# Kernel optimization log

Hardware: AMD Instinct MI355X
Metric: run time of the kernel (lower is better)

## Reference

```python
import jax, jax.numpy as jnp
import numpy as np

D_MODEL = 1024
N_HEADS = 16
HEAD_DIM = D_MODEL // N_HEADS  # 64


def setup_inputs() -> dict:
    key = jax.random.key(0)
    k1, k2, k3 = jax.random.split(key, 3)
    x = jax.random.normal(k1, (2, 2048, D_MODEL), dtype=jnp.float32)
    # nn.Linear(d, 3d, bias=False): store transposed so y = x @ W
    w_qkv = jax.random.normal(k2, (D_MODEL, 3 * D_MODEL), dtype=jnp.float32) * (D_MODEL ** -0.5)
    w_proj = jax.random.normal(k3, (D_MODEL, D_MODEL), dtype=jnp.float32) * (D_MODEL ** -0.5)
    return {"x": x, "w_qkv": w_qkv, "w_proj": w_proj}


def reference(x, w_qkv, w_proj):
    b, n, _ = x.shape
    qkv = x @ w_qkv  # [b, n, 3*d_model]
    # einops 'b n (h d qkv) -> qkv b h n d': qkv axis is innermost of the split
    qkv = qkv.reshape(b, n, N_HEADS, HEAD_DIM, 3)
    q = jnp.moveaxis(qkv[..., 0], 1, 2)  # [b, h, n, d]
    k = jnp.moveaxis(qkv[..., 1], 1, 2)
    v = jnp.moveaxis(qkv[..., 2], 1, 2)
    scale = HEAD_DIM ** -0.5
    scores = jnp.einsum('bhqd,bhkd->bhqk', q, k) * scale  # [b, h, n, n]
    causal = jnp.tril(jnp.ones((n, n), dtype=bool))
    scores = jnp.where(causal[None, None], scores, -jnp.inf)
    attn = jax.nn.softmax(scores, axis=-1)
    out = jnp.einsum('bhqk,bhkd->bhqd', attn, v)  # [b, h, n, d]
    out = jnp.moveaxis(out, 1, 2).reshape(b, n, D_MODEL)  # 'b h n d -> b n (h d)'
    return out @ w_proj
```

## Files before the change

### kernel.cpp

```cpp
#include <hip/hip_runtime.h>
#include <cstdint>
#include <cstddef>

#define D_MODEL 1024
#define N_HEADS 16
#define HEAD_DIM 64
#define SEQ 2048
#define BATCH 2

typedef __attribute__((ext_vector_type(8))) short bf16x8;
typedef __attribute__((ext_vector_type(4))) float f32x4;

__device__ inline unsigned short f2bf(float f) {
    union { float f; unsigned u; } v; v.f = f;
    unsigned r = v.u + 0x7fffu + ((v.u >> 16) & 1u);
    return (unsigned short)(r >> 16);
}

__device__ __forceinline__ unsigned cvtpk_bf16(float lo, float hi) {
    unsigned r;
    asm("v_cvt_pk_bf16_f32 %0, %1, %2" : "=v"(r) : "v"(lo), "v"(hi));
    return r;
}
__device__ __forceinline__ unsigned short f2bf_hw(float f) {
    return (unsigned short)cvtpk_bf16(f, 0.f);
}

__device__ __forceinline__ void gload_lds16(const unsigned short* g, unsigned short* l) {
    __builtin_amdgcn_global_load_lds(
        (const __attribute__((address_space(1))) unsigned int*)g,
        (__attribute__((address_space(3))) unsigned int*)l, 16, 0, 0);
}

#define WAITCNT_VM4 0x0F74
#define WAITCNT_VM0 0x0F70

__global__ __launch_bounds__(256) void fused_convert_kernel(
    const float* __restrict__ X, unsigned short* __restrict__ Xb,
    const float* __restrict__ Wq, unsigned short* __restrict__ Wqt,
    const float* __restrict__ Wp, unsigned short* __restrict__ Wpt)
{
    const int blk = blockIdx.x;
    const int tid = threadIdx.x;
    __shared__ float t[32][33];

    if (blk < 2048) {
        const int idx = blk * 256 + tid;
        const float4* src = (const float4*)X;
        float4 v0 = src[idx * 2], v1 = src[idx * 2 + 1];
        uint4 o;
        o.x = cvtpk_bf16(v0.x, v0.y);
        o.y = cvtpk_bf16(v0.z, v0.w);
        o.z = cvtpk_bf16(v1.x, v1.y);
        o.w = cvtpk_bf16(v1.z, v1.w);
        ((uint4*)Xb)[idx] = o;
    } else if (blk < 5120) {
        const int bb = blk - 2048;
        const int c0 = (bb % 96) * 32, r0 = (bb / 96) * 32;
        const int a = tid & 31, b = tid >> 5;
#pragma unroll
        for (int i = 0; i < 32; i += 8)
            t[b + i][a] = Wq[(size_t)(r0 + b + i) * (3 * D_MODEL) + c0 + a];
        __syncthreads();
#pragma unroll
        for (int i = 0; i < 32; i += 8) {
            const int c = c0 + b + i;
            const int which = c % 3;
            const int np = which * 1024 + c / 3;
            const float s = (which == 0) ? 0.125f : 1.0f;
            Wqt[(size_t)np * D_MODEL + r0 + a] = f2bf_hw(t[a][b + i] * s);
        }
    } else {
        const int bb = blk - 5120;
        const int c0 = (bb % 32) * 32, r0 = (bb / 32) * 32;
        const int a = tid & 31, b = tid >> 5;
#pragma unroll
        for (int i = 0; i < 32; i += 8)
            t[b + i][a] = Wp[(size_t)(r0 + b + i) * D_MODEL + c0 + a];
        __syncthreads();
#pragma unroll
        for (int i = 0; i < 32; i += 8)
            Wpt[(size_t)(c0 + b + i) * D_MODEL + r0 + a] = f2bf_hw(t[a][b + i]);
    }
}

__global__ __launch_bounds__(256) void v_transpose(
    const unsigned short* __restrict__ V, unsigned short* __restrict__ Vt)
{
    const int n0 = blockIdx.x * 64;
    const int bh = blockIdx.y;
    __shared__ unsigned short t[64 * 72];
    const int tid = threadIdx.x;
    const uint4* src = (const uint4*)(V + ((size_t)bh * SEQ + n0) * HEAD_DIM);
#pragma unroll
    for (int it = 0; it < 2; it++) {
        const int lin = tid + it * 256;
        const int row = lin >> 3, p = lin & 7;
        ((uint4*)t)[row * 9 + p] = src[lin];
    }
    __syncthreads();
#pragma unroll
    for (int it = 0; it < 2; it++) {
        const int lin = tid + it * 256;
        const int drow = lin >> 3, p = lin & 7;
        union { unsigned short u[8]; uint4 v; } o;
#pragma unroll
        for (int e = 0; e < 8; e++) o.u[e] = t[(p * 8 + e) * 72 + drow];
        ((uint4*)(Vt + ((size_t)bh * HEAD_DIM + drow) * SEQ + n0))[p] = o.v;
    }
}

#define GEMM_PIPE3_BODY(A_, B_, KBASE, NITER)                                  \
    const int tid = threadIdx.x;                                               \
    const int w = tid >> 6, lane = tid & 63;                                   \
    const int l15 = lane & 15, quad = lane >> 4;                               \
    const int wr = w >> 1, wc = w & 1;                                         \
    const int row0 = blockIdx.y * 128, col0 = blockIdx.x * 128;                \
    __shared__ unsigned short As[3][4096];                                     \
    __shared__ unsigned short Bs[3][4096];                                     \
    const f32x4 zero4 = {0.f, 0.f, 0.f, 0.f};                                  \
    f32x4 acc[4][4];                                                           \
    _Pragma("unroll") for (int i = 0; i < 4; i++)                              \
        _Pragma("unroll") for (int j = 0; j < 4; j++) acc[i][j] = zero4;       \
    auto stage_ = [&](int sb_, int kt_) {                                      \
        const int k0 = (KBASE) + kt_ * 32 + quad * 8;                          \
        _Pragma("unroll") for (int i = 0; i < 2; i++) {                        \
            const int f = w * 2 + i;                                           \
            gload_lds16((A_) + (size_t)(row0 + f * 16 + l15) * D_MODEL + k0,   \
                        &As[sb_][f * 512 + lane * 8]);                         \
            gload_lds16((B_) + (size_t)(col0 + f * 16 + l15) * D_MODEL + k0,   \
                        &Bs[sb_][f * 512 + lane * 8]);                         \
        }                                                                      \
    };                                                                         \
    stage_(0, 0);                                                              \
    stage_(1, 1);                                                              \
    int sb = 0;                                                                \
    for (int kt = 0; kt < (NITER); kt++) {                                     \
        if (kt < (NITER) - 1) {                                                \
            __builtin_amdgcn_s_waitcnt(WAITCNT_VM4);                           \
            __builtin_amdgcn_s_barrier();                                      \
            if (kt + 2 < (NITER)) stage_((sb + 2 > 2) ? sb - 1 : sb + 2, kt + 2); \
        } else {                                                               \
            __builtin_amdgcn_s_waitcnt(WAITCNT_VM0);                           \
            __builtin_amdgcn_s_barrier();                                      \
        }                                                                      \
        bf16x8 af[4], bfr[4];                                                  \
        _Pragma("unroll") for (int i = 0; i < 4; i++)                          \
            af[i] = *(const bf16x8*)&As[sb][(wr * 4 + i) * 512 + lane * 8];    \
        _Pragma("unroll") for (int j = 0; j < 4; j++)                          \
            bfr[j] = *(const bf16x8*)&Bs[sb][(wc * 4 + j) * 512 + lane * 8];   \
        _Pragma("unroll") for (int i = 0; i < 4; i++)                          \
            _Pragma("unroll") for (int j = 0; j < 4; j++)                      \
                acc[i][j] = __builtin_amdgcn_mfma_f32_16x16x32_bf16(           \
                    af[i], bfr[j], acc[i][j], 0, 0, 0);                        \
        sb = (sb == 2) ? 0 : sb + 1;                                           \
    }

__global__ __launch_bounds__(256) void gemm_qkv_mfma(
    const unsigned short* __restrict__ A, const unsigned short* __restrict__ B,
    unsigned short* __restrict__ Q, unsigned short* __restrict__ Kq,
    unsigned short* __restrict__ Vb)
{
    GEMM_PIPE3_BODY(A, B, 0, 32)
    const int nbase = col0 + wc * 64;
    const int which = nbase >> 10;
    unsigned short* const dst = (which == 0) ? Q : (which == 1) ? Kq : Vb;
#pragma unroll
    for (int i = 0; i < 4; i++) {
        const int rowb = row0 + wr * 64 + i * 16 + quad * 4;
        const int bb = rowb >> 11, n = rowb & (SEQ - 1);
#pragma unroll
        for (int rp = 0; rp < 2; rp++) {
#pragma unroll
            for (int j = 0; j < 4; j++) {
                const unsigned u = cvtpk_bf16(acc[i][j][2 * rp], acc[i][j][2 * rp + 1]);
                const int idx = (nbase + j * 16 + l15) & 1023;
                const int h = idx >> 6, dd = idx & 63;
                unsigned short* p =
                    dst + (((size_t)(bb * N_HEADS + h)) * SEQ + n + 2 * rp) * HEAD_DIM + dd;
                p[0] = (unsigned short)u;
                p[HEAD_DIM] = (unsigned short)(u >> 16);
            }
        }
    }
}

__global__ __launch_bounds__(256) void gemm_proj_splitk(
    const unsigned short* __restrict__ A, const unsigned short* __restrict__ B,
    float* __restrict__ P)
{
    const int kbase = blockIdx.z * 512;
    GEMM_PIPE3_BODY(A, B, kbase, 16)
    float* const dst = P + (size_t)blockIdx.z * (4096ull * 1024ull);
#pragma unroll
    for (int i = 0; i < 4; i++) {
#pragma unroll
        for (int r = 0; r < 4; r++) {
            const int row = row0 + wr * 64 + i * 16 + quad * 4 + r;
#pragma unroll
            for (int j = 0; j < 4; j++) {
                const int c = col0 + wc * 64 + j * 16 + l15;
                dst[(size_t)row * D_MODEL + c] = acc[i][j][r];
            }
        }
    }
}

__global__ __launch_bounds__(256) void add_out_kernel(
    const float* __restrict__ P, float* __restrict__ out)
{
    const float4* p0 = (const float4*)P;
    const float4* p1 = (const float4*)(P + 4096ull * 1024ull);
    float4* o = (float4*)out;
    const int base = (blockIdx.x * 256 + threadIdx.x) * 4;
#pragma unroll
    for (int j = 0; j < 4; j++) {
        float4 a = p0[base + j], b = p1[base + j];
        float4 r = {a.x + b.x, a.y + b.y, a.z + b.z, a.w + b.w};
        o[base + j] = r;
    }
}

__global__ __launch_bounds__(256) void flash_attn_kernel(
    const unsigned short* __restrict__ Q,
    const unsigned short* __restrict__ K,
    const unsigned short* __restrict__ Vt,
    unsigned short* __restrict__ O)
{
    const int idx = blockIdx.x;
    const int bh = idx & 31;
    const int qt2 = idx >> 5;
    const int hi = qt2 >> 3, lo = qt2 & 7;
    const int qt = (hi == 0) ? lo : (hi == 1) ? 31 - lo : (hi == 2) ? lo + 8 : 23 - lo;

    const int tid = threadIdx.x;
    const int w = tid >> 6, lane = tid & 63;
    const int l15 = lane & 15, quad = lane >> 4;

    __shared__ unsigned short Ks[2][4096];
    __shared__ unsigned short Vs[2][4096];
    __shared__ unsigned short Ps[4][1024];

    bf16x8 qf[2];
    {
        const unsigned short* qrow =
            Q + ((size_t)bh * SEQ + qt * 64 + w * 16 + l15) * HEAD_DIM;
        qf[0] = *(const bf16x8*)(qrow + quad * 8);
        qf[1] = *(const bf16x8*)(qrow + 32 + quad * 8);
    }

    const f32x4 zero4 = {0.f, 0.f, 0.f, 0.f};
    f32x4 o_acc[4] = {zero4, zero4, zero4, zero4};
    float m_i = -1e30f, l_i = 0.f;

    auto stage = [&](int bf, int kt_t) {
        const int key0 = kt_t * 64;
#pragma unroll
        for (int i = 0; i < 2; i++) {
            const int f = w * 2 + i;
            const int ct = f >> 1, kh = f & 1;
            gload_lds16(K + ((size_t)bh * SEQ + key0 + ct * 16 + l15) * HEAD_DIM
                          + kh * 32 + quad * 8,
                        &Ks[bf][f * 512 + lane * 8]);
            gload_lds16(Vt + ((size_t)bh * HEAD_DIM + ct * 16 + l15) * SEQ
                           + key0 + kh * 32 + quad * 8,
                        &Vs[bf][f * 512 + lane * 8]);
        }
    };

    stage(0, 0);
    int buf = 0;

    const int qg = qt * 64 + w * 16 + l15;

    for (int kt = 0; kt <= qt; kt++) {
        __syncthreads();
        if (kt < qt) stage(buf ^ 1, kt + 1);

        f32x4 st[4] = {zero4, zero4, zero4, zero4};
        __builtin_amdgcn_s_setprio(1);
#pragma unroll
        for (int kh = 0; kh < 2; kh++) {
#pragma unroll
            for (int ct = 0; ct < 4; ct++) {
                bf16x8 kf = *(const bf16x8*)&Ks[buf][(ct * 2 + kh) * 512 + lane * 8];
                st[ct] = __builtin_amdgcn_mfma_f32_16x16x32_bf16(kf, qf[kh], st[ct], 0, 0, 0);
            }
        }
        __builtin_amdgcn_s_setprio(0);

        float mt = -1e30f;
        if (kt == qt) {
#pragma unroll
            for (int ct = 0; ct < 4; ct++) {
#pragma unroll
                for (int r = 0; r < 4; r++) {
                    const int kg = kt * 64 + ct * 16 + quad * 4 + r;
                    float v = (kg > qg) ? -1e30f : st[ct][r];
                    st[ct][r] = v;
                    mt = fmaxf(mt, v);
                }
            }
        } else {
#pragma unroll
            for (int ct = 0; ct < 4; ct++)
#pragma unroll
                for (int r = 0; r < 4; r++)
                    mt = fmaxf(mt, st[ct][r]);
        }
        mt = fmaxf(mt, __shfl_xor(mt, 16));
        mt = fmaxf(mt, __shfl_xor(mt, 32));

        float mn = m_i;
        if (!__all(mt <= m_i + 8.0f)) {
            mn = fmaxf(m_i, mt);
            const float alpha = __expf(m_i - mn);
            m_i = mn;
            l_i *= alpha;
            float ar[4];
#pragma unroll
            for (int r = 0; r < 4; r++)
                ar[r] = __shfl(alpha, (lane & 48) | (quad * 4 + r));
#pragma unroll
            for (int dt = 0; dt < 4; dt++)
#pragma unroll
                for (int r = 0; r < 4; r++)
                    o_acc[dt][r] *= ar[r];
        }

        float ls = 0.f;
#pragma unroll
        for (int ct = 0; ct < 4; ct++) {
            const float p0 = __expf(st[ct][0] - mn);
            const float p1 = __expf(st[ct][1] - mn);
            const float p2 = __expf(st[ct][2] - mn);
            const float p3 = __expf(st[ct][3] - mn);
            ls += (p0 + p1) + (p2 + p3);
            uint2 pk2;
            pk2.x = cvtpk_bf16(p0, p1);
            pk2.y = cvtpk_bf16(p2, p3);
            const int addr = (ct >> 1) * 512 + ((ct & 1) * 2 + (quad >> 1)) * 128
                           + l15 * 8 + (quad & 1) * 4;
            *(uint2*)&Ps[w][addr] = pk2;
        }
        l_i += ls;

        __builtin_amdgcn_s_setprio(1);
#pragma unroll
        for (int kh = 0; kh < 2; kh++) {
            bf16x8 pa = *(const bf16x8*)&Ps[w][kh * 512 + quad * 128 + l15 * 8];
#pragma unroll
            for (int dt = 0; dt < 4; dt++) {
                bf16x8 vf = *(const bf16x8*)&Vs[buf][(dt * 2 + kh) * 512 + lane * 8];
                o_acc[dt] = __builtin_amdgcn_mfma_f32_16x16x32_bf16(pa, vf, o_acc[dt], 0, 0, 0);
            }
        }
        __builtin_amdgcn_s_setprio(0);
        buf ^= 1;
    }

    l_i += __shfl_xor(l_i, 16);
    l_i += __shfl_xor(l_i, 32);
    const float linv = 1.0f / l_i;
    float lr[4];
#pragma unroll
    for (int r = 0; r < 4; r++)
        lr[r] = __shfl(linv, (lane & 48) | (quad * 4 + r));

    const int b = bh >> 4, h = bh & 15;
#pragma unroll
    for (int r = 0; r < 4; r++) {
        const int q = qt * 64 + w * 16 + quad * 4 + r;
        unsigned short* orow = O + ((size_t)b * SEQ + q) * D_MODEL + h * HEAD_DIM;
#pragma unroll
        for (int dt = 0; dt < 4; dt++)
            orow[dt * 16 + l15] = f2bf_hw(o_acc[dt][r] * lr[r]);
    }
}

extern "C" void kernel_launch(void* const* d_in, const int* in_sizes, int n_in,
                              void* d_out, int out_size, void* d_ws, size_t ws_size,
                              hipStream_t stream) {
    const float* x      = (const float*)d_in[0];
    const float* w_qkv  = (const float*)d_in[1];
    const float* w_proj = (const float*)d_in[2];
    float* out = (float*)d_out;

    unsigned short* Xb  = (unsigned short*)d_ws;
    unsigned short* Wqt = Xb  + (size_t)4 * 1024 * 1024;
    unsigned short* Wpt = Wqt + (size_t)3 * 1024 * 1024;
    unsigned short* Qb  = Wpt + (size_t)1 * 1024 * 1024;
    unsigned short* Kb  = Qb  + (size_t)4 * 1024 * 1024;
    unsigned short* Vb  = Kb  + (size_t)4 * 1024 * 1024;
    unsigned short* Vtb = Vb  + (size_t)4 * 1024 * 1024;
    unsigned short* Ob  = Vtb + (size_t)4 * 1024 * 1024;

    float* Pp = (float*)Qb;

    fused_convert_kernel<<<dim3(6144), 256, 0, stream>>>(
        x, Xb, w_qkv, Wqt, w_proj, Wpt);

    gemm_qkv_mfma<<<dim3(3 * D_MODEL / 128, BATCH * SEQ / 128), 256, 0, stream>>>(
        Xb, Wqt, Qb, Kb, Vb);

    v_transpose<<<dim3(SEQ / 64, BATCH * N_HEADS), 256, 0, stream>>>(Vb, Vtb);

    flash_attn_kernel<<<dim3(SEQ / 64 * BATCH * N_HEADS), 256, 0, stream>>>(
        Qb, Kb, Vtb, Ob);

    gemm_proj_splitk<<<dim3(D_MODEL / 128, BATCH * SEQ / 128, 2), 256, 0, stream>>>(
        Ob, Wpt, Pp);

    add_out_kernel<<<dim3(1024), 256, 0, stream>>>(Pp, out);
}
```

Baseline: 217.2 us.

## Retile GEMMs to 128x64 with 2 waves, double buffering, XCD-aware block swizzle

Both GEMMs change from 128x128 tiles with 4 waves and a 3-stage LDS pipeline to 128x64 tiles with 2 waves (each wave owns 64 rows) and a 2-stage double buffer. Block indices are remapped so each XCD gets a contiguous region of the output grid for better L2 locality. The smaller tile and LDS footprint are meant to raise occupancy and block count and to simplify the per-head epilogue. In exchange, each tile reuses less data, and waiting on all outstanding loads every iteration reduces load/compute overlap.

```diff
diff --git a/kernel.cpp b/kernel.cpp
--- a/kernel.cpp
+++ b/kernel.cpp
@@ -32,7 +32,6 @@
         (__attribute__((address_space(3))) unsigned int*)l, 16, 0, 0);
 }
 
-#define WAITCNT_VM4 0x0F74
 #define WAITCNT_VM0 0x0F70
 
 __global__ __launch_bounds__(256) void fused_convert_kernel(
@@ -110,74 +109,72 @@
     }
 }
 
-#define GEMM_PIPE3_BODY(A_, B_, KBASE, NITER)                                  \
+#define GEMM_PIPE2_BODY(A_, B_, KBASE, NITER, BX_, BY_)                        \
     const int tid = threadIdx.x;                                               \
     const int w = tid >> 6, lane = tid & 63;                                   \
     const int l15 = lane & 15, quad = lane >> 4;                               \
-    const int wr = w >> 1, wc = w & 1;                                         \
-    const int row0 = blockIdx.y * 128, col0 = blockIdx.x * 128;                \
-    __shared__ unsigned short As[3][4096];                                     \
-    __shared__ unsigned short Bs[3][4096];                                     \
+    const int row0 = (BY_) * 128, col0 = (BX_) * 64;                           \
+    __shared__ unsigned short SM_[12288];     \
     const f32x4 zero4 = {0.f, 0.f, 0.f, 0.f};                                  \
     f32x4 acc[4][4];                                                           \
     _Pragma("unroll") for (int i = 0; i < 4; i++)                              \
         _Pragma("unroll") for (int j = 0; j < 4; j++) acc[i][j] = zero4;       \
     auto stage_ = [&](int sb_, int kt_) {                                      \
         const int k0 = (KBASE) + kt_ * 32 + quad * 8;                          \
+        _Pragma("unroll") for (int i = 0; i < 4; i++) {                        \
+            const int f = w * 4 + i;                                           \
+            gload_lds16((A_) + (size_t)(row0 + f * 16 + l15) * D_MODEL + k0,   \
+                        &SM_[sb_ * 4096 + f * 512 + lane * 8]);                \
+        }                                                                      \
         _Pragma("unroll") for (int i = 0; i < 2; i++) {                        \
-            const int f = w * 2 + i;                                           \
-            gload_lds16((A_) + (size_t)(row0 + f * 16 + l15) * D_MODEL + k0,   \
-                        &As[sb_][f * 512 + lane * 8]);                         \
-            gload_lds16((B_) + (size_t)(col0 + f * 16 + l15) * D_MODEL + k0,   \
-                        &Bs[sb_][f * 512 + lane * 8]);                         \
+            const int g = w * 2 + i;                                           \
+            gload_lds16((B_) + (size_t)(col0 + g * 16 + l15) * D_MODEL + k0,   \
+                        &SM_[8192 + sb_ * 2048 + g * 512 + lane * 8]);         \
         }                                                                      \
     };                                                                         \
     stage_(0, 0);                                                              \
-    stage_(1, 1);                                                              \
     int sb = 0;                                                                \
     for (int kt = 0; kt < (NITER); kt++) {                                     \
-        if (kt < (NITER) - 1) {                                                \
-            __builtin_amdgcn_s_waitcnt(WAITCNT_VM4);                           \
-            __builtin_amdgcn_s_barrier();                                      \
-            if (kt + 2 < (NITER)) stage_((sb + 2 > 2) ? sb - 1 : sb + 2, kt + 2); \
-        } else {                                                               \
-            __builtin_amdgcn_s_waitcnt(WAITCNT_VM0);                           \
-            __builtin_amdgcn_s_barrier();                                      \
-        }                                                                      \
+        __builtin_amdgcn_s_waitcnt(WAITCNT_VM0);                               \
+        __builtin_amdgcn_s_barrier();                                          \
+        if (kt + 1 < (NITER)) stage_(sb ^ 1, kt + 1);                          \
         bf16x8 af[4], bfr[4];                                                  \
         _Pragma("unroll") for (int i = 0; i < 4; i++)                          \
-            af[i] = *(const bf16x8*)&As[sb][(wr * 4 + i) * 512 + lane * 8];    \
+            af[i] = *(const bf16x8*)&SM_[sb * 4096 + (w * 4 + i) * 512 + lane * 8]; \
         _Pragma("unroll") for (int j = 0; j < 4; j++)                          \
-            bfr[j] = *(const bf16x8*)&Bs[sb][(wc * 4 + j) * 512 + lane * 8];   \
+            bfr[j] = *(const bf16x8*)&SM_[8192 + sb * 2048 + j * 512 + lane * 8];   \
         _Pragma("unroll") for (int i = 0; i < 4; i++)                          \
             _Pragma("unroll") for (int j = 0; j < 4; j++)                      \
                 acc[i][j] = __builtin_amdgcn_mfma_f32_16x16x32_bf16(           \
                     af[i], bfr[j], acc[i][j], 0, 0, 0);                        \
-        sb = (sb == 2) ? 0 : sb + 1;                                           \
-    }
-
-__global__ __launch_bounds__(256) void gemm_qkv_mfma(
+        sb ^= 1;                                                               \
+    }
+
+__global__ __launch_bounds__(128) void gemm_qkv_mfma(
     const unsigned short* __restrict__ A, const unsigned short* __restrict__ B,
     unsigned short* __restrict__ Q, unsigned short* __restrict__ Kq,
     unsigned short* __restrict__ Vb)
 {
-    GEMM_PIPE3_BODY(A, B, 0, 32)
-    const int nbase = col0 + wc * 64;
-    const int which = nbase >> 10;
+    const int lin = blockIdx.x + 48 * blockIdx.y;
+    const int xcd = lin & 7, t = lin >> 3;
+    const int bx = (xcd & 1) * 24 + t % 24;
+    const int by = (xcd >> 1) * 8 + t / 24;
+    GEMM_PIPE2_BODY(A, B, 0, 32, bx, by)
+    const int which = col0 >> 10;
+    const int hloc = (col0 >> 6) & 15;
     unsigned short* const dst = (which == 0) ? Q : (which == 1) ? Kq : Vb;
 #pragma unroll
     for (int i = 0; i < 4; i++) {
-        const int rowb = row0 + wr * 64 + i * 16 + quad * 4;
+        const int rowb = row0 + w * 64 + i * 16 + quad * 4;
         const int bb = rowb >> 11, n = rowb & (SEQ - 1);
 #pragma unroll
         for (int rp = 0; rp < 2; rp++) {
 #pragma unroll
             for (int j = 0; j < 4; j++) {
                 const unsigned u = cvtpk_bf16(acc[i][j][2 * rp], acc[i][j][2 * rp + 1]);
-                const int idx = (nbase + j * 16 + l15) & 1023;
-                const int h = idx >> 6, dd = idx & 63;
+                const int dd = j * 16 + l15;
                 unsigned short* p =
-                    dst + (((size_t)(bb * N_HEADS + h)) * SEQ + n + 2 * rp) * HEAD_DIM + dd;
+                    dst + (((size_t)(bb * N_HEADS + hloc)) * SEQ + n + 2 * rp) * HEAD_DIM + dd;
                 p[0] = (unsigned short)u;
                 p[HEAD_DIM] = (unsigned short)(u >> 16);
             }
@@ -185,21 +182,25 @@
     }
 }
 
-__global__ __launch_bounds__(256) void gemm_proj_splitk(
+__global__ __launch_bounds__(128) void gemm_proj_splitk(
     const unsigned short* __restrict__ A, const unsigned short* __restrict__ B,
     float* __restrict__ P)
 {
+    const int lin = blockIdx.x + 16 * blockIdx.y;
+    const int xcd = lin & 7, t = lin >> 3;
+    const int bx = (xcd & 1) * 8 + t % 8;
+    const int by = (xcd >> 1) * 8 + t / 8;
     const int kbase = blockIdx.z * 512;
-    GEMM_PIPE3_BODY(A, B, kbase, 16)
+    GEMM_PIPE2_BODY(A, B, kbase, 16, bx, by)
     float* const dst = P + (size_t)blockIdx.z * (4096ull * 1024ull);
 #pragma unroll
     for (int i = 0; i < 4; i++) {
 #pragma unroll
         for (int r = 0; r < 4; r++) {
-            const int row = row0 + wr * 64 + i * 16 + quad * 4 + r;
+            const int row = row0 + w * 64 + i * 16 + quad * 4 + r;
 #pragma unroll
             for (int j = 0; j < 4; j++) {
-                const int c = col0 + wc * 64 + j * 16 + l15;
+                const int c = col0 + j * 16 + l15;
                 dst[(size_t)row * D_MODEL + c] = acc[i][j][r];
             }
         }
@@ -400,7 +401,7 @@
     fused_convert_kernel<<<dim3(6144), 256, 0, stream>>>(
         x, Xb, w_qkv, Wqt, w_proj, Wpt);
 
-    gemm_qkv_mfma<<<dim3(3 * D_MODEL / 128, BATCH * SEQ / 128), 256, 0, stream>>>(
+    gemm_qkv_mfma<<<dim3(48, 32), 128, 0, stream>>>(
         Xb, Wqt, Qb, Kb, Vb);
 
     v_transpose<<<dim3(SEQ / 64, BATCH * N_HEADS), 256, 0, stream>>>(Vb, Vtb);
@@ -408,7 +409,7 @@
     flash_attn_kernel<<<dim3(SEQ / 64 * BATCH * N_HEADS), 256, 0, stream>>>(
         Qb, Kb, Vtb, Ob);
 
-    gemm_proj_splitk<<<dim3(D_MODEL / 128, BATCH * SEQ / 128, 2), 256, 0, stream>>>(
+    gemm_proj_splitk<<<dim3(16, 32, 2), 128, 0, stream>>>(
         Ob, Wpt, Pp);
 
     add_out_kernel<<<dim3(1024), 256, 0, stream>>>(Pp, out);
```

After: 241.9 us. 11.4% more time.
